# Kernel optimization log

Measured on AMD Instinct MI355X. Metric: run time of the kernel, lower is better.

## Reference

```python
import jax, jax.numpy as jnp
import numpy as np

M = 5  # neighbours per down point (M_i = 5 when n_up > 5)


def _per_graph(h, s_l, scores, W_emb, b_emb):
    # h: [N,H], s_l: [N,3], scores: [N]
    N, H = h.shape
    n_up = N // 4  # floor(0.25 * N)
    top_idx = jnp.argsort(-scores)[:n_up]
    up_mask = jnp.zeros((N,), bool).at[top_idx].set(True)
    up_idx = jnp.sort(top_idx)                     # up nodes in ascending node order
    down_idx = jnp.argsort(up_mask)[: N - n_up]    # stable: down nodes ascending

    # embedding_features_to_att: Linear(H+4 -> H) on concat(h, s_l, scores)
    feat = jnp.concatenate([h, s_l, scores[:, None]], axis=1) @ W_emb + b_emb  # [N,H]

    # directional KNN: for each down point, M nearest up points in 3D coords
    d2 = jnp.sum((s_l[down_idx][:, None, :] - s_l[up_idx][None, :, :]) ** 2, -1)  # [Nd,Nu]
    _, nn_local = jax.lax.top_k(-d2, M)            # [Nd,M] indices into up set
    dst = up_idx[nn_local].reshape(-1)             # edge destinations (up nodes)
    src = jnp.repeat(down_idx, M)                  # edge sources (down nodes)

    # DGL update_all: copy src 'features' -> max reduce at dst; no-msg nodes = 0
    msgs = feat[src]                               # [Nd*M, H]
    out = jnp.full((N, H), -jnp.inf, feat.dtype).at[dst].max(msgs)
    out = jnp.where(jnp.isneginf(out), jnp.zeros((), feat.dtype), out)
    return out, up_mask


def setup_inputs() -> dict:
    key = jax.random.key(0)
    k1, k2, k3, k4, k5 = jax.random.split(key, 5)
    B, N, H = 8, 8192, 256
    return {
        "h": jax.random.normal(k1, (B, N, H), jnp.float32),
        "s_l": jax.random.normal(k2, (B, N, 3), jnp.float32),
        "scores": jax.random.uniform(k3, (B, N), jnp.float32),
        "W_emb": jax.random.normal(k4, (H + 4, H), jnp.float32) * 0.02,
        "b_emb": jax.random.normal(k5, (H,), jnp.float32) * 0.02,
    }


def reference(h, s_l, scores, W_emb, b_emb):
    out, up_mask = jax.vmap(_per_graph, in_axes=(0, 0, 0, None, None))(
        h, s_l, scores, W_emb, b_emb)
    B, N, H = out.shape
    return out.reshape(B * N, H), up_mask.reshape(-1)
```

## Files before the change

### kernel.cpp

```cpp
#include <hip/hip_runtime.h>

#define Bb 8
#define Nn 8192
#define Hh 256
#define NUP 2048
#define NDOWN (Nn - NUP)
#define MM 5
#define EPB (NDOWN * MM)
#define KP 288
#define LDA 36
#define LSTW 17

typedef short v8s __attribute__((ext_vector_type(8)));
typedef float v4f __attribute__((ext_vector_type(4)));

__device__ __forceinline__ unsigned short bfc(float f) {
    unsigned u = __float_as_uint(f);
    return (unsigned short)((u + 0x7FFFu + ((u >> 16) & 1u)) >> 16);
}

template <int NB>
__device__ void find_kth_bin(const int* hist, int kth, int tid,
                             int* wsumA, int* res, int* out_bin, int* out_cntgt) {
    constexpr int PER = NB / 1024;
    int ln = tid & 63, wv = tid >> 6;
    int b0 = NB - 1 - PER * tid;
    int c0 = hist[b0];
    int c1 = (PER == 2) ? hist[b0 - 1] : 0;
    int tot = c0 + c1;
    int x = tot;
    #pragma unroll
    for (int off = 1; off < 64; off <<= 1) {
        int y = __shfl_up(x, off);
        if (ln >= off) x += y;
    }
    if (ln == 63) wsumA[wv] = x;
    __syncthreads();
    int wbase = 0;
    for (int w = 0; w < wv; w++) wbase += wsumA[w];
    int excl = wbase + x - tot;
    if (excl < kth && excl + c0 >= kth) { res[0] = b0; res[1] = excl; }
    else if (PER == 2 && excl + c0 < kth && excl + c0 + c1 >= kth) { res[0] = b0 - 1; res[1] = excl + c0; }
    __syncthreads();
    *out_bin = res[0];
    *out_cntgt = res[1];
}

__global__ __launch_bounds__(1024) void select_kernel(
        const float* __restrict__ scores, const float* __restrict__ sl,
        int* __restrict__ mask, float4* __restrict__ upc,
        float4* __restrict__ dnc, int* __restrict__ deg) {
    int b = blockIdx.x;
    int tid = threadIdx.x;
    int ln = tid & 63, wv = tid >> 6;
    __shared__ int hist[2048];
    __shared__ int wsumA[16];
    __shared__ int res[2];
    const float* s = scores + (size_t)b * Nn;

    deg[b * NUP + tid] = 0;
    deg[b * NUP + 1024 + tid] = 0;

    float4 sa = *(const float4*)(s + tid * 8);
    float4 sb = *(const float4*)(s + tid * 8 + 4);
    unsigned ub[8] = {__float_as_uint(sa.x), __float_as_uint(sa.y),
                      __float_as_uint(sa.z), __float_as_uint(sa.w),
                      __float_as_uint(sb.x), __float_as_uint(sb.y),
                      __float_as_uint(sb.z), __float_as_uint(sb.w)};

    hist[tid] = 0; hist[tid + 1024] = 0;
    __syncthreads();
    #pragma unroll
    for (int k = 0; k < 8; k++) atomicAdd(&hist[ub[k] >> 21], 1);
    __syncthreads();
    int B1, gt1;
    find_kth_bin<2048>(hist, NUP, tid, wsumA, res, &B1, &gt1);
    int slots1 = NUP - gt1;

    hist[tid] = 0; hist[tid + 1024] = 0;
    __syncthreads();
    #pragma unroll
    for (int k = 0; k < 8; k++)
        if ((int)(ub[k] >> 21) == B1) atomicAdd(&hist[(ub[k] >> 10) & 0x7FF], 1);
    __syncthreads();
    int B2, gt2;
    find_kth_bin<2048>(hist, slots1, tid, wsumA, res, &B2, &gt2);
    int slots2 = slots1 - gt2;
    unsigned hi22 = ((unsigned)B1 << 11) | (unsigned)B2;

    hist[tid] = 0; hist[tid + 1024] = 0;
    __syncthreads();
    #pragma unroll
    for (int k = 0; k < 8; k++)
        if ((ub[k] >> 10) == hi22) atomicAdd(&hist[ub[k] & 0x3FF], 1);
    __syncthreads();
    int B3, gt3;
    find_kth_bin<1024>(hist, slots2, tid, wsumA, res, &B3, &gt3);
    int slots_eq = slots2 - gt3;
    unsigned T = (hi22 << 10) | (unsigned)B3;

    int eqc = 0;
    #pragma unroll
    for (int k = 0; k < 8; k++) eqc += (ub[k] == T) ? 1 : 0;
    int x = eqc;
    #pragma unroll
    for (int off = 1; off < 64; off <<= 1) {
        int y = __shfl_up(x, off);
        if (ln >= off) x += y;
    }
    if (ln == 63) wsumA[wv] = x;
    __syncthreads();
    int eqb = x - eqc;
    for (int w = 0; w < wv; w++) eqb += wsumA[w];
    __syncthreads();

    int upcnt = 0, eqrun = 0, upf = 0;
    #pragma unroll
    for (int k = 0; k < 8; k++) {
        bool eq = (ub[k] == T);
        bool up = (ub[k] > T) || (eq && (eqb + eqrun) < slots_eq);
        eqrun += eq ? 1 : 0;
        upf |= (up ? 1 : 0) << k;
        upcnt += up ? 1 : 0;
    }
    x = upcnt;
    #pragma unroll
    for (int off = 1; off < 64; off <<= 1) {
        int y = __shfl_up(x, off);
        if (ln >= off) x += y;
    }
    if (ln == 63) wsumA[wv] = x;
    __syncthreads();
    int upb = x - upcnt;
    for (int w = 0; w < wv; w++) upb += wsumA[w];

    int uprun = 0;
    #pragma unroll
    for (int k = 0; k < 8; k++) {
        int node = tid * 8 + k;
        int g = b * Nn + node;
        float4 c;
        c.x = sl[(size_t)g * 3 + 0];
        c.y = sl[(size_t)g * 3 + 1];
        c.z = sl[(size_t)g * 3 + 2];
        c.w = __int_as_float(node);
        bool up = (upf >> k) & 1;
        if (up) upc[b * NUP + upb + uprun] = c;
        else    dnc[b * NDOWN + node - (upb + uprun)] = c;
        mask[g] = up ? 1 : 0;
        uprun += up ? 1 : 0;
    }
}

__global__ __launch_bounds__(512) void knn_brute(
        const float4* __restrict__ upc, const float4* __restrict__ dnc,
        int* __restrict__ knn, int* __restrict__ deg) {
    int b = blockIdx.y;
    int tid = threadIdx.x;
    int sub = tid >> 6, dn = tid & 63;
    __shared__ float xs[NUP], ys[NUP], zs[NUP];
    __shared__ unsigned long long Ubuf[1312];
    __shared__ int lcnt[64];
    float* sF = (float*)Ubuf;
    unsigned long long* lst = Ubuf + 32;

    float4 d = dnc[b * NDOWN + blockIdx.x * 64 + dn];
    float xd = d.x, yd = d.y, zd = d.z;
    int node = __float_as_int(d.w);

    const float4* U = upc + b * NUP;
    #pragma unroll
    for (int q = 0; q < 4; q++) {
        int i = q * 512 + tid;
        float4 u = U[i];
        xs[i] = u.x; ys[i] = u.y; zs[i] = u.z;
    }
    if (tid < 64) lcnt[tid] = 0;
    __syncthreads();

    float L0 = 3.4e38f, L1 = 3.4e38f, L2 = 3.4e38f, L3 = 3.4e38f, L4 = 3.4e38f;
    const int j0 = sub * 256;
    #pragma unroll 4
    for (int j = j0; j < j0 + 256; ++j) {
        float dx = xs[j] - xd, dy = ys[j] - yd, dz = zs[j] - zd;
        float d2 = fmaf(dx, dx, fmaf(dy, dy, dz * dz));
        L4 = __builtin_amdgcn_fmed3f(d2, L3, L4);
        L3 = __builtin_amdgcn_fmed3f(d2, L2, L3);
        L2 = __builtin_amdgcn_fmed3f(d2, L1, L2);
        L1 = __builtin_amdgcn_fmed3f(d2, L0, L1);
        L0 = fminf(d2, L0);
    }
    sF[(sub * MM + 0) * 64 + dn] = L0;
    sF[(sub * MM + 1) * 64 + dn] = L1;
    sF[(sub * MM + 2) * 64 + dn] = L2;
    sF[(sub * MM + 3) * 64 + dn] = L3;
    sF[(sub * MM + 4) * 64 + dn] = L4;
    __syncthreads();

    if (sub == 0) {
        float F0 = 3.4e38f, F1 = 3.4e38f, F2 = 3.4e38f, F3 = 3.4e38f, F4 = 3.4e38f;
        for (int l = 0; l < 8; l++) {
            #pragma unroll
            for (int m = 0; m < MM; m++) {
                float v = sF[(l * MM + m) * 64 + dn];
                F4 = __builtin_amdgcn_fmed3f(v, F3, F4);
                F3 = __builtin_amdgcn_fmed3f(v, F2, F3);
                F2 = __builtin_amdgcn_fmed3f(v, F1, F2);
                F1 = __builtin_amdgcn_fmed3f(v, F0, F1);
                F0 = fminf(v, F0);
            }
        }
        sF[dn] = F4;
    }
    __syncthreads();
    float thr = sF[dn];

    #pragma unroll 4
    for (int j = j0; j < j0 + 256; ++j) {
        float dx = xs[j] - xd, dy = ys[j] - yd, dz = zs[j] - zd;
        float d2 = fmaf(dx, dx, fmaf(dy, dy, dz * dz));
        if (d2 <= thr) {
            unsigned long long key =
                ((unsigned long long)__float_as_uint(d2) << 32) |
                (unsigned long long)(unsigned)j;
            int s = atomicAdd(&lcnt[dn], 1);
            if (s < LSTW - 1) lst[dn * LSTW + s] = key;
        }
    }
    __syncthreads();

    if (sub == 0) {
        unsigned long long fin[MM];
        #pragma unroll
        for (int m = 0; m < MM; m++) fin[m] = 0xFFFFFFFFFFFFFFFFull;
        int n = min(lcnt[dn], LSTW - 1);
        for (int s = 0; s < n; s++) {
            unsigned long long cand = lst[dn * LSTW + s];
            #pragma unroll
            for (int m = 0; m < MM; m++) {
                bool lt = cand < fin[m];
                unsigned long long lo = lt ? cand : fin[m];
                unsigned long long hi = lt ? fin[m] : cand;
                fin[m] = lo; cand = hi;
            }
        }
        int g = b * Nn + node;
        #pragma unroll
        for (int m = 0; m < MM; m++) {
            int lid = (int)(unsigned)(fin[m] & 0xFFFFFFFFull);
            knn[g * MM + m] = lid;
            atomicAdd(&deg[b * NUP + lid], 1);
        }
    }
}

__global__ void wt_kernel(const float* __restrict__ W, const float* __restrict__ bias,
                          unsigned short* __restrict__ Wt) {
    int n = blockIdx.x;
    int k = threadIdx.x;
    Wt[n * KP + k] = bfc(W[(size_t)k * Hh + n]);
    if (k < KP - 256) {
        int kk = 256 + k;
        unsigned short v = 0;
        if (kk < 260)       v = bfc(W[(size_t)kk * Hh + n]);
        else if (kk == 260) v = bfc(bias[n]);
        Wt[n * KP + kk] = v;
    }
}

__global__ void feat_mfma(const float* __restrict__ h, const float* __restrict__ sl,
                          const float* __restrict__ sc, const unsigned short* __restrict__ Wt,
                          const float4* __restrict__ dnc, float* __restrict__ out) {
    int b = blockIdx.z;
    int m0 = blockIdx.x * 128;
    int n0 = blockIdx.y * 128;
    int tid = threadIdx.x;
    __shared__ unsigned short Al[128 * LDA];
    __shared__ unsigned short Bl[128 * LDA];
    __shared__ int ndid[128];
    int wid = tid >> 6, lane = tid & 63;
    int wm = (wid & 1) * 64, wn = (wid >> 1) * 64;
    int lm = lane & 15, quad = lane >> 4;
    if (tid < 128) ndid[tid] = __float_as_int(dnc[b * NDOWN + m0 + tid].w);
    v4f acc[4][4];
    #pragma unroll
    for (int i = 0; i < 4; i++)
        #pragma unroll
        for (int j = 0; j < 4; j++)
            acc[i][j] = (v4f){0.f, 0.f, 0.f, 0.f};
    const float* hb = h + (size_t)b * Nn * Hh;
    for (int t = 0; t < 9; t++) {
        int k0 = t * 32;
        __syncthreads();
        if (t < 8) {
            #pragma unroll
            for (int q = 0; q < 4; q++) {
                int e = q * 256 + tid;
                int row = e >> 3, kq = e & 7;
                float4 v = *(const float4*)(hb + (size_t)ndid[row] * Hh + k0 + kq * 4);
                ushort4 o = make_ushort4(bfc(v.x), bfc(v.y), bfc(v.z), bfc(v.w));
                *(ushort4*)(Al + row * LDA + kq * 4) = o;
            }
        } else if (tid < 128) {
            int row = tid;
            int g = b * Nn + ndid[row];
            unsigned short r[32];
            #pragma unroll
            for (int k = 0; k < 32; k++) r[k] = 0;
            r[0] = bfc(sl[(size_t)g * 3 + 0]);
            r[1] = bfc(sl[(size_t)g * 3 + 1]);
            r[2] = bfc(sl[(size_t)g * 3 + 2]);
            r[3] = bfc(sc[g]);
            r[4] = 0x3F80;
            #pragma unroll
            for (int q = 0; q < 8; q++)
                *(ushort4*)(Al + row * LDA + q * 4) =
                    make_ushort4(r[q * 4], r[q * 4 + 1], r[q * 4 + 2], r[q * 4 + 3]);
        }
        #pragma unroll
        for (int q = 0; q < 4; q++) {
            int e = q * 256 + tid;
            int n = e >> 3, kq = e & 7;
            ushort4 v = *(const ushort4*)(Wt + (size_t)(n0 + n) * KP + k0 + kq * 4);
            *(ushort4*)(Bl + n * LDA + kq * 4) = v;
        }
        __syncthreads();
        v8s af[4], bfr[4];
        #pragma unroll
        for (int i = 0; i < 4; i++)
            af[i] = *(const v8s*)(Al + (wm + i * 16 + lm) * LDA + quad * 8);
        #pragma unroll
        for (int j = 0; j < 4; j++)
            bfr[j] = *(const v8s*)(Bl + (wn + j * 16 + lm) * LDA + quad * 8);
        #pragma unroll
        for (int i = 0; i < 4; i++)
            #pragma unroll
            for (int j = 0; j < 4; j++)
                acc[i][j] = __builtin_amdgcn_mfma_f32_16x16x32_bf16(af[i], bfr[j], acc[i][j], 0, 0, 0);
    }
    #pragma unroll
    for (int i = 0; i < 4; i++) {
        #pragma unroll
        for (int r = 0; r < 4; r++) {
            int lrow = wm + i * 16 + quad * 4 + r;
            size_t base = ((size_t)b * Nn + ndid[lrow]) * Hh + n0 + wn + lm;
            #pragma unroll
            for (int j = 0; j < 4; j++)
                out[base + j * 16] = acc[i][j][r];
        }
    }
}

__global__ __launch_bounds__(1024) void csr_scan(const int* __restrict__ deg,
                                                 int* __restrict__ rowptr,
                                                 int* __restrict__ cursor) {
    int b = blockIdx.x;
    int tid = threadIdx.x;
    int ln = tid & 63, wv = tid >> 6;
    __shared__ int wsum[16];
    int d0 = deg[b * NUP + 2 * tid], d1 = deg[b * NUP + 2 * tid + 1];
    int s = d0 + d1;
    int x = s;
    #pragma unroll
    for (int off = 1; off < 64; off <<= 1) {
        int y = __shfl_up(x, off);
        if (ln >= off) x += y;
    }
    if (ln == 63) wsum[wv] = x;
    __syncthreads();
    int base = 0;
    for (int w = 0; w < wv; w++) base += wsum[w];
    int excl = base + x - s;
    rowptr[b * (NUP + 1) + 2 * tid] = excl;
    rowptr[b * (NUP + 1) + 2 * tid + 1] = excl + d0;
    cursor[b * NUP + 2 * tid] = excl;
    cursor[b * NUP + 2 * tid + 1] = excl + d0;
    if (tid == 1023) rowptr[b * (NUP + 1) + NUP] = excl + s;
}

__global__ void csr_fill(const float4* __restrict__ dnc, const int* __restrict__ knn,
                         int* __restrict__ cursor, int* __restrict__ edges) {
    int b = blockIdx.y;
    int r = blockIdx.x * 256 + threadIdx.x;
    int node = __float_as_int(dnc[b * NDOWN + r].w);
    int g = b * Nn + node;
    #pragma unroll
    for (int m = 0; m < MM; m++) {
        int un = knn[g * MM + m];
        int slot = atomicAdd(&cursor[b * NUP + un], 1);
        edges[b * EPB + slot] = node;
    }
}

__global__ void gather_kernel(const float4* __restrict__ upc, const int* __restrict__ rowptr,
                              const int* __restrict__ edges, float* __restrict__ out) {
    int b = blockIdx.y;
    int u = blockIdx.x * 4 + (threadIdx.x >> 6);
    int lane = threadIdx.x & 63;
    int node = __float_as_int(upc[b * NUP + u].w);
    int start = rowptr[b * (NUP + 1) + u];
    int end   = rowptr[b * (NUP + 1) + u + 1];
    const int* eb = edges + b * EPB;
    size_t rowbase = (size_t)b * Nn * Hh + (size_t)(lane << 2);
    float4 a0 = make_float4(-3.4e38f, -3.4e38f, -3.4e38f, -3.4e38f);
    float4 a1 = a0, a2 = a0, a3 = a0;
    int e = start;
    for (; e + 4 <= end; e += 4) {
        int s0 = eb[e], s1 = eb[e + 1], s2 = eb[e + 2], s3 = eb[e + 3];
        float4 v0 = *(const float4*)(out + rowbase + (size_t)s0 * Hh);
        float4 v1 = *(const float4*)(out + rowbase + (size_t)s1 * Hh);
        float4 v2 = *(const float4*)(out + rowbase + (size_t)s2 * Hh);
        float4 v3 = *(const float4*)(out + rowbase + (size_t)s3 * Hh);
        a0.x = fmaxf(a0.x, v0.x); a0.y = fmaxf(a0.y, v0.y);
        a0.z = fmaxf(a0.z, v0.z); a0.w = fmaxf(a0.w, v0.w);
        a1.x = fmaxf(a1.x, v1.x); a1.y = fmaxf(a1.y, v1.y);
        a1.z = fmaxf(a1.z, v1.z); a1.w = fmaxf(a1.w, v1.w);
        a2.x = fmaxf(a2.x, v2.x); a2.y = fmaxf(a2.y, v2.y);
        a2.z = fmaxf(a2.z, v2.z); a2.w = fmaxf(a2.w, v2.w);
        a3.x = fmaxf(a3.x, v3.x); a3.y = fmaxf(a3.y, v3.y);
        a3.z = fmaxf(a3.z, v3.z); a3.w = fmaxf(a3.w, v3.w);
    }
    for (; e < end; e++) {
        int s0 = eb[e];
        float4 v0 = *(const float4*)(out + rowbase + (size_t)s0 * Hh);
        a0.x = fmaxf(a0.x, v0.x); a0.y = fmaxf(a0.y, v0.y);
        a0.z = fmaxf(a0.z, v0.z); a0.w = fmaxf(a0.w, v0.w);
    }
    float4 r;
    r.x = fmaxf(fmaxf(a0.x, a1.x), fmaxf(a2.x, a3.x));
    r.y = fmaxf(fmaxf(a0.y, a1.y), fmaxf(a2.y, a3.y));
    r.z = fmaxf(fmaxf(a0.z, a1.z), fmaxf(a2.z, a3.z));
    r.w = fmaxf(fmaxf(a0.w, a1.w), fmaxf(a2.w, a3.w));
    if (start == end) r = make_float4(0.f, 0.f, 0.f, 0.f);
    *(float4*)(out + rowbase + (size_t)node * Hh) = r;
}

__global__ void finalize_kernel(const int* __restrict__ mask, float* __restrict__ out) {
    int b = blockIdx.y;
    int node = blockIdx.x * 4 + (threadIdx.x >> 6);
    int g = b * Nn + node;
    int lane = threadIdx.x & 63;
    bool up = mask[g] != 0;
    if (!up)
        *(float4*)(out + (size_t)g * Hh + (lane << 2)) = make_float4(0.f, 0.f, 0.f, 0.f);
    if (lane == 0) out[(size_t)Bb * Nn * Hh + g] = up ? 1.0f : 0.0f;
}

extern "C" void kernel_launch(void* const* d_in, const int* in_sizes, int n_in,
                              void* d_out, int out_size, void* d_ws, size_t ws_size,
                              hipStream_t stream) {
    const float* h    = (const float*)d_in[0];
    const float* sl   = (const float*)d_in[1];
    const float* sc   = (const float*)d_in[2];
    const float* W    = (const float*)d_in[3];
    const float* bias = (const float*)d_in[4];

    char* ws = (char*)d_ws;
    int* mask = (int*)ws;                 ws += (size_t)Bb * Nn * sizeof(int);
    int* knn  = (int*)ws;                 ws += (size_t)Bb * Nn * MM * sizeof(int);
    float4* upc = (float4*)ws;            ws += (size_t)Bb * NUP * sizeof(float4);
    float4* dnc = (float4*)ws;            ws += (size_t)Bb * NDOWN * sizeof(float4);
    unsigned short* Wt = (unsigned short*)ws; ws += (size_t)Hh * KP * sizeof(unsigned short);
    int* deg = (int*)ws;                  ws += (size_t)Bb * NUP * sizeof(int);
    int* cursor = (int*)ws;               ws += (size_t)Bb * NUP * sizeof(int);
    int* rowptr = (int*)ws;               ws += (size_t)Bb * (NUP + 1) * sizeof(int);
    int* edges = (int*)ws;
    float* outf = (float*)d_out;

    dim3 blk(256);
    select_kernel<<<dim3(Bb), dim3(1024), 0, stream>>>(sc, sl, mask, upc, dnc, deg);
    knn_brute<<<dim3(NDOWN / 64, Bb), dim3(512), 0, stream>>>(upc, dnc, knn, deg);
    csr_scan<<<dim3(Bb), dim3(1024), 0, stream>>>(deg, rowptr, cursor);
    csr_fill<<<dim3(NDOWN / 256, Bb), blk, 0, stream>>>(dnc, knn, cursor, edges);
    wt_kernel<<<dim3(Hh), blk, 0, stream>>>(W, bias, Wt);
    feat_mfma<<<dim3(NDOWN / 128, 2, Bb), blk, 0, stream>>>(h, sl, sc, Wt, dnc, outf);
    gather_kernel<<<dim3(NUP / 4, Bb), blk, 0, stream>>>(upc, rowptr, edges, outf);
    finalize_kernel<<<dim3(Nn / 4, Bb), blk, 0, stream>>>(mask, outf);
}
```

Baseline: 264.5 us.

## Use expanded-norm distance in KNN, vectorise coord loads, drop mask buffer

The first KNN pass now reads packed float4 coordinates, each carrying its precomputed squared norm, and ranks candidates with a partial distance (|u|^2 - 2u·d). The candidate threshold is widened by a small epsilon to absorb the rounding of this form, and the candidate list width grows to hold the extra entries. The select kernel loads the 24 coordinate floats per thread with vector loads and no longer writes a mask array. Mask output now comes from the gather kernel for up nodes and from a zero_down kernel that touches only down rows, so finalize no longer scans every node. The risks are extra threshold candidates from the epsilon and possible list overflow in dense regions.

```diff
diff --git a/kernel.cpp b/kernel.cpp
--- a/kernel.cpp
+++ b/kernel.cpp
@@ -9,7 +9,7 @@
 #define EPB (NDOWN * MM)
 #define KP 288
 #define LDA 36
-#define LSTW 17
+#define LSTW 20
 
 typedef short v8s __attribute__((ext_vector_type(8)));
 typedef float v4f __attribute__((ext_vector_type(4)));
@@ -48,8 +48,8 @@
 
 __global__ __launch_bounds__(1024) void select_kernel(
         const float* __restrict__ scores, const float* __restrict__ sl,
-        int* __restrict__ mask, float4* __restrict__ upc,
-        float4* __restrict__ dnc, int* __restrict__ deg) {
+        float4* __restrict__ upc, float4* __restrict__ dnc,
+        int* __restrict__ deg) {
     int b = blockIdx.x;
     int tid = threadIdx.x;
     int ln = tid & 63, wv = tid >> 6;
@@ -134,20 +134,25 @@
     int upb = x - upcnt;
     for (int w = 0; w < wv; w++) upb += wsumA[w];
 
+    const float* slb = sl + ((size_t)b * Nn + (size_t)tid * 8) * 3;
+    float fb[24];
+    *(float4*)(fb + 0)  = *(const float4*)(slb + 0);
+    *(float4*)(fb + 4)  = *(const float4*)(slb + 4);
+    *(float4*)(fb + 8)  = *(const float4*)(slb + 8);
+    *(float4*)(fb + 12) = *(const float4*)(slb + 12);
+    *(float4*)(fb + 16) = *(const float4*)(slb + 16);
+    *(float4*)(fb + 20) = *(const float4*)(slb + 20);
+
     int uprun = 0;
     #pragma unroll
     for (int k = 0; k < 8; k++) {
         int node = tid * 8 + k;
-        int g = b * Nn + node;
         float4 c;
-        c.x = sl[(size_t)g * 3 + 0];
-        c.y = sl[(size_t)g * 3 + 1];
-        c.z = sl[(size_t)g * 3 + 2];
+        c.x = fb[3 * k]; c.y = fb[3 * k + 1]; c.z = fb[3 * k + 2];
         c.w = __int_as_float(node);
         bool up = (upf >> k) & 1;
         if (up) upc[b * NUP + upb + uprun] = c;
         else    dnc[b * NDOWN + node - (upb + uprun)] = c;
-        mask[g] = up ? 1 : 0;
         uprun += up ? 1 : 0;
     }
 }
@@ -158,7 +163,7 @@
     int b = blockIdx.y;
     int tid = threadIdx.x;
     int sub = tid >> 6, dn = tid & 63;
-    __shared__ float xs[NUP], ys[NUP], zs[NUP];
+    __shared__ float4 stage[NUP];
     __shared__ unsigned long long Ubuf[1312];
     __shared__ int lcnt[64];
     float* sF = (float*)Ubuf;
@@ -167,13 +172,16 @@
     float4 d = dnc[b * NDOWN + blockIdx.x * 64 + dn];
     float xd = d.x, yd = d.y, zd = d.z;
     int node = __float_as_int(d.w);
+    float c1 = -2.0f * xd, c2 = -2.0f * yd, c3 = -2.0f * zd;
+    float kd = fmaf(xd, xd, fmaf(yd, yd, zd * zd));
 
     const float4* U = upc + b * NUP;
     #pragma unroll
     for (int q = 0; q < 4; q++) {
         int i = q * 512 + tid;
         float4 u = U[i];
-        xs[i] = u.x; ys[i] = u.y; zs[i] = u.z;
+        u.w = fmaf(u.x, u.x, fmaf(u.y, u.y, u.z * u.z));
+        stage[i] = u;
     }
     if (tid < 64) lcnt[tid] = 0;
     __syncthreads();
@@ -182,13 +190,13 @@
     const int j0 = sub * 256;
     #pragma unroll 4
     for (int j = j0; j < j0 + 256; ++j) {
-        float dx = xs[j] - xd, dy = ys[j] - yd, dz = zs[j] - zd;
-        float d2 = fmaf(dx, dx, fmaf(dy, dy, dz * dz));
-        L4 = __builtin_amdgcn_fmed3f(d2, L3, L4);
-        L3 = __builtin_amdgcn_fmed3f(d2, L2, L3);
-        L2 = __builtin_amdgcn_fmed3f(d2, L1, L2);
-        L1 = __builtin_amdgcn_fmed3f(d2, L0, L1);
-        L0 = fminf(d2, L0);
+        float4 c = stage[j];
+        float t = fmaf(c.x, c1, fmaf(c.y, c2, fmaf(c.z, c3, c.w)));
+        L4 = __builtin_amdgcn_fmed3f(t, L3, L4);
+        L3 = __builtin_amdgcn_fmed3f(t, L2, L3);
+        L2 = __builtin_amdgcn_fmed3f(t, L1, L2);
+        L1 = __builtin_amdgcn_fmed3f(t, L0, L1);
+        L0 = fminf(t, L0);
     }
     sF[(sub * MM + 0) * 64 + dn] = L0;
     sF[(sub * MM + 1) * 64 + dn] = L1;
@@ -213,11 +221,12 @@
         sF[dn] = F4;
     }
     __syncthreads();
-    float thr = sF[dn];
+    float thr = sF[dn] + kd + 1e-3f;
 
     #pragma unroll 4
     for (int j = j0; j < j0 + 256; ++j) {
-        float dx = xs[j] - xd, dy = ys[j] - yd, dz = zs[j] - zd;
+        float4 c = stage[j];
+        float dx = c.x - xd, dy = c.y - yd, dz = c.z - zd;
         float d2 = fmaf(dx, dx, fmaf(dy, dy, dz * dz));
         if (d2 <= thr) {
             unsigned long long key =
@@ -433,17 +442,17 @@
     r.w = fmaxf(fmaxf(a0.w, a1.w), fmaxf(a2.w, a3.w));
     if (start == end) r = make_float4(0.f, 0.f, 0.f, 0.f);
     *(float4*)(out + rowbase + (size_t)node * Hh) = r;
-}
-
-__global__ void finalize_kernel(const int* __restrict__ mask, float* __restrict__ out) {
+    if (lane == 0) out[(size_t)Bb * Nn * Hh + b * Nn + node] = 1.0f;
+}
+
+__global__ void zero_down(const float4* __restrict__ dnc, float* __restrict__ out) {
     int b = blockIdx.y;
-    int node = blockIdx.x * 4 + (threadIdx.x >> 6);
+    int r = blockIdx.x * 4 + (threadIdx.x >> 6);
+    int lane = threadIdx.x & 63;
+    int node = __float_as_int(dnc[b * NDOWN + r].w);
     int g = b * Nn + node;
-    int lane = threadIdx.x & 63;
-    bool up = mask[g] != 0;
-    if (!up)
-        *(float4*)(out + (size_t)g * Hh + (lane << 2)) = make_float4(0.f, 0.f, 0.f, 0.f);
-    if (lane == 0) out[(size_t)Bb * Nn * Hh + g] = up ? 1.0f : 0.0f;
+    *(float4*)(out + (size_t)g * Hh + (lane << 2)) = make_float4(0.f, 0.f, 0.f, 0.f);
+    if (lane == 0) out[(size_t)Bb * Nn * Hh + g] = 0.0f;
 }
 
 extern "C" void kernel_launch(void* const* d_in, const int* in_sizes, int n_in,
@@ -456,7 +465,6 @@
     const float* bias = (const float*)d_in[4];
 
     char* ws = (char*)d_ws;
-    int* mask = (int*)ws;                 ws += (size_t)Bb * Nn * sizeof(int);
     int* knn  = (int*)ws;                 ws += (size_t)Bb * Nn * MM * sizeof(int);
     float4* upc = (float4*)ws;            ws += (size_t)Bb * NUP * sizeof(float4);
     float4* dnc = (float4*)ws;            ws += (size_t)Bb * NDOWN * sizeof(float4);
@@ -468,12 +476,12 @@
     float* outf = (float*)d_out;
 
     dim3 blk(256);
-    select_kernel<<<dim3(Bb), dim3(1024), 0, stream>>>(sc, sl, mask, upc, dnc, deg);
+    select_kernel<<<dim3(Bb), dim3(1024), 0, stream>>>(sc, sl, upc, dnc, deg);
     knn_brute<<<dim3(NDOWN / 64, Bb), dim3(512), 0, stream>>>(upc, dnc, knn, deg);
     csr_scan<<<dim3(Bb), dim3(1024), 0, stream>>>(deg, rowptr, cursor);
     csr_fill<<<dim3(NDOWN / 256, Bb), blk, 0, stream>>>(dnc, knn, cursor, edges);
     wt_kernel<<<dim3(Hh), blk, 0, stream>>>(W, bias, Wt);
     feat_mfma<<<dim3(NDOWN / 128, 2, Bb), blk, 0, stream>>>(h, sl, sc, Wt, dnc, outf);
     gather_kernel<<<dim3(NUP / 4, Bb), blk, 0, stream>>>(upc, rowptr, edges, outf);
-    finalize_kernel<<<dim3(Nn / 4, Bb), blk, 0, stream>>>(mask, outf);
-}
+    zero_down<<<dim3(NDOWN / 4, Bb), blk, 0, stream>>>(dnc, outf);
+}
```

After: 263.0 us. About the same (-0.6%).
